# Kernel optimization log

Hardware: AMD Instinct MI355X
Metric: run time of the kernel (lower is better)

## Reference

```python
import jax, jax.numpy as jnp
import numpy as np

POOL_SIZE = 7
NUM_ROIS = 1024
H, W, C = 256, 256, 512


def setup_inputs() -> dict:
    key = jax.random.key(0)
    k_img, k_xy, k_wh = jax.random.split(key, 3)
    img = jax.random.normal(k_img, (1, H, W, C), dtype=jnp.float32)
    # Valid ROIs: top-left in [0, 192), size in [8, 64), clipped to image bounds.
    xy = jax.random.randint(k_xy, (1, NUM_ROIS, 2), 0, 192)          # (x1, y1)
    wh = jax.random.randint(k_wh, (1, NUM_ROIS, 2), 8, 64)           # (w, h)
    x1y1 = xy
    x2y2 = jnp.minimum(xy + wh, jnp.array([W, H]))
    rois = jnp.concatenate([x1y1, x2y2], axis=-1).astype(jnp.int32)  # [1, R, 4] = (x1, y1, x2, y2)
    return {"img": img, "rois": rois}


def _roi_resize(feat, roi, P):
    """Bilinear-resize crop feat[y1:y2, x1:x2, :] to (P, P) — TF1 legacy mapping.
    feat: [H, W, C] float, roi: [4] int32 (x1, y1, x2, y2). Returns [P, P, C]."""
    x1, y1, x2, y2 = roi[0], roi[1], roi[2], roi[3]
    h = (y2 - y1).astype(jnp.float32)
    w = (x2 - x1).astype(jnp.float32)
    # src coordinate (crop-relative) = out_idx * (in_size / out_size)
    ys = jnp.arange(P, dtype=jnp.float32) * (h / P)   # [P]
    xs = jnp.arange(P, dtype=jnp.float32) * (w / P)   # [P]
    y0 = jnp.floor(ys).astype(jnp.int32)
    x0 = jnp.floor(xs).astype(jnp.int32)
    y1i = jnp.minimum(y0 + 1, jnp.maximum(y2 - y1 - 1, 0))
    x1i = jnp.minimum(x0 + 1, jnp.maximum(x2 - x1 - 1, 0))
    wy = (ys - y0.astype(jnp.float32))[:, None, None]  # [P,1,1]
    wx = (xs - x0.astype(jnp.float32))[None, :, None]  # [1,P,1]
    r0, r1 = y1 + y0, y1 + y1i                         # absolute rows
    c0, c1 = x1 + x0, x1 + x1i                         # absolute cols
    v00 = feat[r0[:, None], c0[None, :], :]            # [P,P,C]
    v01 = feat[r0[:, None], c1[None, :], :]
    v10 = feat[r1[:, None], c0[None, :], :]
    v11 = feat[r1[:, None], c1[None, :], :]
    return (v00 * (1.0 - wy) * (1.0 - wx) + v01 * (1.0 - wy) * wx
            + v10 * wy * (1.0 - wx) + v11 * wy * wx)


def reference(img, rois):
    feat = img[0]                                       # [H, W, C]
    pooled = jax.vmap(_roi_resize, in_axes=(None, 0, None))(feat, rois[0], POOL_SIZE)
    return pooled[None]                                 # [1, num_rois, P, P, C]
```

## Files before the change

### kernel.cpp

```cpp
#include <hip/hip_runtime.h>

#define POOL 7
#define IMG_H 256
#define IMG_W 256
#define IMG_C 512
#define NUM_ROIS 1024

__global__ __launch_bounds__(128) void roi_pool_kernel(
    const float* __restrict__ img,
    const int*   __restrict__ rois,
    float*       __restrict__ out)
{
    const int cell = blockIdx.x;
    const int roi  = blockIdx.y;
    const int py = cell / POOL;
    const int px = cell - py * POOL;

    const int4 rb = ((const int4*)rois)[roi];
    const int x1 = rb.x, y1 = rb.y, x2 = rb.z, y2 = rb.w;

    const float h = (float)(y2 - y1);
    const float w = (float)(x2 - x1);
    const float ys = (float)py * (h * (1.0f / POOL));
    const float xs = (float)px * (w * (1.0f / POOL));
    const int y0 = (int)floorf(ys);
    const int x0 = (int)floorf(xs);
    const int y1i = min(y0 + 1, max(y2 - y1 - 1, 0));
    const int x1i = min(x0 + 1, max(x2 - x1 - 1, 0));
    const float wy = ys - (float)y0;
    const float wx = xs - (float)x0;

    const int r0 = y1 + y0,  r1 = y1 + y1i;
    const int c0 = x1 + x0,  c1 = x1 + x1i;

    const float w00 = (1.0f - wy) * (1.0f - wx);
    const float w01 = (1.0f - wy) * wx;
    const float w10 = wy * (1.0f - wx);
    const float w11 = wy * wx;

    const float4* p00 = (const float4*)(img + ((size_t)r0 * IMG_W + c0) * IMG_C);
    const float4* p01 = (const float4*)(img + ((size_t)r0 * IMG_W + c1) * IMG_C);
    const float4* p10 = (const float4*)(img + ((size_t)r1 * IMG_W + c0) * IMG_C);
    const float4* p11 = (const float4*)(img + ((size_t)r1 * IMG_W + c1) * IMG_C);
    float4* po = (float4*)(out + (((size_t)roi * POOL + py) * POOL + px) * IMG_C);

    const int t = threadIdx.x;
    const float4 v00 = p00[t];
    const float4 v01 = p01[t];
    const float4 v10 = p10[t];
    const float4 v11 = p11[t];

    float4 o;
    o.x = v00.x * w00 + v01.x * w01 + v10.x * w10 + v11.x * w11;
    o.y = v00.y * w00 + v01.y * w01 + v10.y * w10 + v11.y * w11;
    o.z = v00.z * w00 + v01.z * w01 + v10.z * w10 + v11.z * w11;
    o.w = v00.w * w00 + v01.w * w01 + v10.w * w10 + v11.w * w11;
    po[t] = o;
}

extern "C" void kernel_launch(void* const* d_in, const int* in_sizes, int n_in,
                              void* d_out, int out_size, void* d_ws, size_t ws_size,
                              hipStream_t stream) {
    const float* img  = (const float*)d_in[0];
    const int*   rois = (const int*)d_in[1];
    float* out = (float*)d_out;

    dim3 grid(POOL * POOL, NUM_ROIS);
    dim3 block(128);
    roi_pool_kernel<<<grid, block, 0, stream>>>(img, rois, out);
}
```

Baseline: 238.8 us.

## Process a full output row per block with XCD-aware ROI mapping and nontemporal stores

Each block now computes all 7 columns of one pooled row instead of a single cell, so the grid shrinks sevenfold and the ROI and row setup is paid once per row. Block IDs are remapped so that consecutive blocks, which are dispatched round-robin across the 8 XCDs, place all blocks of one ROI on the same XCD to improve L2 reuse of the shared image rows. Output writes use nontemporal stores to avoid polluting cache, and the ROI fields are made scalar with readfirstlane. The trade-off is fewer blocks in flight and more serial work per thread.

Result: no change. 236.5 us (-0.9%).

```diff
diff --git a/kernel.cpp b/kernel.cpp
--- a/kernel.cpp
+++ b/kernel.cpp
@@ -1,61 +1,70 @@
 #include <hip/hip_runtime.h>
 
 #define POOL 7
-#define IMG_H 256
 #define IMG_W 256
 #define IMG_C 512
 #define NUM_ROIS 1024
+
+typedef float f4 __attribute__((ext_vector_type(4)));
 
 __global__ __launch_bounds__(128) void roi_pool_kernel(
     const float* __restrict__ img,
     const int*   __restrict__ rois,
     float*       __restrict__ out)
 {
-    const int cell = blockIdx.x;
-    const int roi  = blockIdx.y;
-    const int py = cell / POOL;
-    const int px = cell - py * POOL;
+    const int bid  = blockIdx.x;
+    const int xcd  = bid & 7;
+    const int slot = bid >> 3;
+    const int rloc = slot / POOL;
+    const int py   = slot - rloc * POOL;
+    const int roi  = xcd * (NUM_ROIS / 8) + rloc;
 
     const int4 rb = ((const int4*)rois)[roi];
-    const int x1 = rb.x, y1 = rb.y, x2 = rb.z, y2 = rb.w;
+    const int x1 = __builtin_amdgcn_readfirstlane(rb.x);
+    const int y1 = __builtin_amdgcn_readfirstlane(rb.y);
+    const int x2 = __builtin_amdgcn_readfirstlane(rb.z);
+    const int y2 = __builtin_amdgcn_readfirstlane(rb.w);
 
     const float h = (float)(y2 - y1);
     const float w = (float)(x2 - x1);
-    const float ys = (float)py * (h * (1.0f / POOL));
-    const float xs = (float)px * (w * (1.0f / POOL));
-    const int y0 = (int)floorf(ys);
-    const int x0 = (int)floorf(xs);
-    const int y1i = min(y0 + 1, max(y2 - y1 - 1, 0));
-    const int x1i = min(x0 + 1, max(x2 - x1 - 1, 0));
+    const float sy = h / (float)POOL;
+    const float sx = w / (float)POOL;
+
+    const float ys = (float)py * sy;
+    const int   y0 = (int)floorf(ys);
+    const int   y1i = min(y0 + 1, max(y2 - y1 - 1, 0));
     const float wy = ys - (float)y0;
-    const float wx = xs - (float)x0;
 
-    const int r0 = y1 + y0,  r1 = y1 + y1i;
-    const int c0 = x1 + x0,  c1 = x1 + x1i;
-
-    const float w00 = (1.0f - wy) * (1.0f - wx);
-    const float w01 = (1.0f - wy) * wx;
-    const float w10 = wy * (1.0f - wx);
-    const float w11 = wy * wx;
-
-    const float4* p00 = (const float4*)(img + ((size_t)r0 * IMG_W + c0) * IMG_C);
-    const float4* p01 = (const float4*)(img + ((size_t)r0 * IMG_W + c1) * IMG_C);
-    const float4* p10 = (const float4*)(img + ((size_t)r1 * IMG_W + c0) * IMG_C);
-    const float4* p11 = (const float4*)(img + ((size_t)r1 * IMG_W + c1) * IMG_C);
-    float4* po = (float4*)(out + (((size_t)roi * POOL + py) * POOL + px) * IMG_C);
+    const size_t rowstride = (size_t)IMG_W * IMG_C;
+    const float* row0 = img + (size_t)(y1 + y0)  * rowstride;
+    const float* row1 = img + (size_t)(y1 + y1i) * rowstride;
 
     const int t = threadIdx.x;
-    const float4 v00 = p00[t];
-    const float4 v01 = p01[t];
-    const float4 v10 = p10[t];
-    const float4 v11 = p11[t];
+    f4* obase = (f4*)out + ((size_t)roi * (POOL * POOL) + (size_t)py * POOL) * (IMG_C / 4) + t;
 
-    float4 o;
-    o.x = v00.x * w00 + v01.x * w01 + v10.x * w10 + v11.x * w11;
-    o.y = v00.y * w00 + v01.y * w01 + v10.y * w10 + v11.y * w11;
-    o.z = v00.z * w00 + v01.z * w01 + v10.z * w10 + v11.z * w11;
-    o.w = v00.w * w00 + v01.w * w01 + v10.w * w10 + v11.w * w11;
-    po[t] = o;
+    const int cmax = max(x2 - x1 - 1, 0);
+
+#pragma unroll
+    for (int px = 0; px < POOL; ++px) {
+        const float xs = (float)px * sx;
+        const int   x0 = (int)floorf(xs);
+        const int   x1i = min(x0 + 1, cmax);
+        const float wx = xs - (float)x0;
+        const int c0 = x1 + x0, c1 = x1 + x1i;
+
+        const f4 v00 = ((const f4*)(row0 + (size_t)c0 * IMG_C))[t];
+        const f4 v01 = ((const f4*)(row0 + (size_t)c1 * IMG_C))[t];
+        const f4 v10 = ((const f4*)(row1 + (size_t)c0 * IMG_C))[t];
+        const f4 v11 = ((const f4*)(row1 + (size_t)c1 * IMG_C))[t];
+
+        const float w00 = (1.0f - wy) * (1.0f - wx);
+        const float w01 = (1.0f - wy) * wx;
+        const float w10 = wy * (1.0f - wx);
+        const float w11 = wy * wx;
+
+        f4 o = v00 * w00 + v01 * w01 + v10 * w10 + v11 * w11;
+        __builtin_nontemporal_store(o, obase + px * (IMG_C / 4));
+    }
 }
 
 extern "C" void kernel_launch(void* const* d_in, const int* in_sizes, int n_in,
@@ -65,7 +74,7 @@
     const int*   rois = (const int*)d_in[1];
     float* out = (float*)d_out;
 
-    dim3 grid(POOL * POOL, NUM_ROIS);
+    dim3 grid(NUM_ROIS * POOL);
     dim3 block(128);
     roi_pool_kernel<<<grid, block, 0, stream>>>(img, rois, out);
 }
```
